# Optimization experiments

Hardware: AMD Instinct MI355X
Metric: run time of the kernel (lower is better)

Reference implementation:

```python
import jax, jax.numpy as jnp
import numpy as np

N_NODES = 40000
N_EDGES = 640000
D_IN = 128
D_OUT = 128


def setup_inputs() -> dict:
    key = jax.random.key(0)
    k_feat, k_src, k_dst, k_ws, k_wn = jax.random.split(key, 5)
    feat = jax.random.normal(k_feat, (N_NODES, D_IN), dtype=jnp.float32)
    src = jax.random.randint(k_src, (N_EDGES,), 0, N_NODES, dtype=jnp.int32)
    dst = jax.random.randint(k_dst, (N_EDGES,), 0, N_NODES, dtype=jnp.int32)
    # Glorot-ish init for the two dense layers
    scale = 1.0 / np.sqrt(D_IN)
    W_self = jax.random.normal(k_ws, (D_IN, D_OUT), dtype=jnp.float32) * scale
    W_neigh = jax.random.normal(k_wn, (D_IN, D_OUT), dtype=jnp.float32) * scale
    b_self = jnp.zeros((D_OUT,), dtype=jnp.float32)
    b_neigh = jnp.zeros((D_OUT,), dtype=jnp.float32)
    return {"feat": feat, "src": src, "dst": dst,
            "W_self": W_self, "b_self": b_self,
            "W_neigh": W_neigh, "b_neigh": b_neigh}


def reference(feat, src, dst, W_self, b_self, W_neigh, b_neigh):
    # --- mean aggregation: copy_src('h','m') + mean('m','neigh') ---
    # Gather source features along edges, segment-sum into dst, divide by in-degree.
    msgs = feat[src]  # [E, D_in]
    neigh_sum = jax.ops.segment_sum(msgs, dst, num_segments=N_NODES)  # [N, D_in]
    deg = jax.ops.segment_sum(jnp.ones((src.shape[0],), feat.dtype), dst,
                              num_segments=N_NODES)  # [N]
    # DGL mean reducer yields 0 for nodes with no incoming edges.
    h_neigh = neigh_sum / jnp.maximum(deg, 1.0)[:, None]
    # --- fc_self(h_self) + fc_neigh(h_neigh) ---
    rst = (feat @ W_self + b_self) + (h_neigh @ W_neigh + b_neigh)
    return rst
```

## Files before the change

### kernel.cpp

```cpp
#include <hip/hip_runtime.h>
#include <cstddef>

constexpr int NN  = 40000;
constexpr int NE  = 640000;
constexpr int DIM = 128;
constexpr int CAP = 48;
constexpr int PLANE = NN * 64;

typedef __attribute__((ext_vector_type(8))) short short8;
typedef __attribute__((ext_vector_type(4))) float floatx4;
typedef __attribute__((ext_vector_type(4))) unsigned int uint32x4;

__device__ __forceinline__ unsigned short f2bf(float x) {
    union { float f; unsigned int i; } v; v.f = x;
    unsigned int u = v.i;
    return (unsigned short)((u + 0x7fffu + ((u >> 16) & 1u)) >> 16);
}
__device__ __forceinline__ float bflo2f(unsigned int u) {
    union { unsigned int i; float f; } v; v.i = u << 16; return v.f;
}
__device__ __forceinline__ float bfhi2f(unsigned int u) {
    union { unsigned int i; float f; } v; v.i = u & 0xffff0000u; return v.f;
}

__global__ __launch_bounds__(256) void k_prep(
    const float* __restrict__ feat, const float* __restrict__ Wself,
    const float* __restrict__ Wneigh, unsigned short* __restrict__ featb,
    unsigned short* __restrict__ Wc, int* __restrict__ cnt)
{
    int b = blockIdx.x, t = threadIdx.x;
    if (b < 2500) {
        int idx8 = b * 256 + t;
        int n  = idx8 >> 4;
        int d0 = (idx8 & 15) << 3;
        const float4* fp =
            reinterpret_cast<const float4*>(feat + (size_t)n * DIM + d0);
        float4 v0 = fp[0], v1 = fp[1];
        unsigned int p0 = (unsigned int)f2bf(v0.x) | ((unsigned int)f2bf(v0.y) << 16);
        unsigned int p1 = (unsigned int)f2bf(v0.z) | ((unsigned int)f2bf(v0.w) << 16);
        unsigned int p2 = (unsigned int)f2bf(v1.x) | ((unsigned int)f2bf(v1.y) << 16);
        unsigned int p3 = (unsigned int)f2bf(v1.z) | ((unsigned int)f2bf(v1.w) << 16);
        int plane = d0 >> 6, off = d0 & 63;
        *reinterpret_cast<uint4*>(
            featb + (size_t)plane * PLANE + (size_t)n * 64 + off) =
            make_uint4(p0, p1, p2, p3);
    } else if (b < 2628) {
        int idx = (b - 2500) * 256 + t;
        int c = idx >> 13, n = (idx >> 6) & 127, kp = idx & 63;
        int k = c * 64 + kp;
        float w = (k < DIM) ? Wself[(size_t)k * DIM + n]
                            : Wneigh[(size_t)(k - DIM) * DIM + n];
        Wc[idx] = f2bf(w);
    } else {
        int i = (b - 2628) * 256 + t;
        if (i < NN) cnt[i] = 0;
    }
}

__global__ __launch_bounds__(256) void k_fill(
    const int* __restrict__ src, const int* __restrict__ dst,
    int* __restrict__ cnt, unsigned short* __restrict__ colf)
{
    int r  = blockIdx.x & 7;
    int bi = blockIdx.x >> 3;
    int lo = r * 5000, hi = lo + 5000;
    const uint32x4* d4 = reinterpret_cast<const uint32x4*>(dst) + (size_t)bi * 2000;
    const uint32x4* s4 = reinterpret_cast<const uint32x4*>(src) + (size_t)bi * 2000;
    for (int it = threadIdx.x; it < 2000; it += 256) {
        uint32x4 dv = __builtin_nontemporal_load(d4 + it);
        uint32x4 sv = __builtin_nontemporal_load(s4 + it);
        #pragma unroll
        for (int k = 0; k < 4; ++k) {
            int d = (int)dv[k];
            if (d >= lo && d < hi) {
                int pos = atomicAdd(&cnt[d], 1);
                if (pos < CAP) colf[d * CAP + pos] = (unsigned short)sv[k];
            }
        }
    }
}

__global__ __launch_bounds__(256) void k_gather(
    const unsigned int* __restrict__ fb32,
    const int* __restrict__ cnt,
    const unsigned short* __restrict__ colf,
    unsigned int* __restrict__ hnb32)
{
    int gtid = blockIdx.x * blockDim.x + threadIdx.x;
    int n = gtid >> 6;
    if (n >= NN) return;
    int lane = threadIdx.x & 63;

    int deg = cnt[n];
    int m = min(deg, CAP);
    int sv = (lane < m) ? (int)colf[n * CAP + lane] : 0;

    int vb = (lane >> 5) * (NN * 32) + (lane & 31);
    float ax0 = 0.f, ay0 = 0.f, ax1 = 0.f, ay1 = 0.f;
    int i = 0;
    for (; i + 7 < m; i += 8) {
        int s0 = __shfl(sv, i),     s1 = __shfl(sv, i + 1);
        int s2 = __shfl(sv, i + 2), s3 = __shfl(sv, i + 3);
        int s4 = __shfl(sv, i + 4), s5 = __shfl(sv, i + 5);
        int s6 = __shfl(sv, i + 6), s7 = __shfl(sv, i + 7);
        unsigned int u0 = fb32[vb + s0 * 32];
        unsigned int u1 = fb32[vb + s1 * 32];
        unsigned int u2 = fb32[vb + s2 * 32];
        unsigned int u3 = fb32[vb + s3 * 32];
        unsigned int u4 = fb32[vb + s4 * 32];
        unsigned int u5 = fb32[vb + s5 * 32];
        unsigned int u6 = fb32[vb + s6 * 32];
        unsigned int u7 = fb32[vb + s7 * 32];
        ax0 += bflo2f(u0); ay0 += bfhi2f(u0);
        ax1 += bflo2f(u1); ay1 += bfhi2f(u1);
        ax0 += bflo2f(u2); ay0 += bfhi2f(u2);
        ax1 += bflo2f(u3); ay1 += bfhi2f(u3);
        ax0 += bflo2f(u4); ay0 += bfhi2f(u4);
        ax1 += bflo2f(u5); ay1 += bfhi2f(u5);
        ax0 += bflo2f(u6); ay0 += bfhi2f(u6);
        ax1 += bflo2f(u7); ay1 += bfhi2f(u7);
    }
    for (; i + 3 < m; i += 4) {
        int s0 = __shfl(sv, i),     s1 = __shfl(sv, i + 1);
        int s2 = __shfl(sv, i + 2), s3 = __shfl(sv, i + 3);
        unsigned int u0 = fb32[vb + s0 * 32];
        unsigned int u1 = fb32[vb + s1 * 32];
        unsigned int u2 = fb32[vb + s2 * 32];
        unsigned int u3 = fb32[vb + s3 * 32];
        ax0 += bflo2f(u0); ay0 += bfhi2f(u0);
        ax1 += bflo2f(u1); ay1 += bfhi2f(u1);
        ax0 += bflo2f(u2); ay0 += bfhi2f(u2);
        ax1 += bflo2f(u3); ay1 += bfhi2f(u3);
    }
    for (; i < m; ++i) {
        int s0 = __shfl(sv, i);
        unsigned int u0 = fb32[vb + s0 * 32];
        ax0 += bflo2f(u0); ay0 += bfhi2f(u0);
    }
    float inv = 1.0f / fmaxf((float)deg, 1.0f);
    float ax = (ax0 + ax1) * inv, ay = (ay0 + ay1) * inv;
    hnb32[vb + n * 32] = (unsigned int)f2bf(ax) | ((unsigned int)f2bf(ay) << 16);
}

__global__ __launch_bounds__(320) void k_gemm(
    const unsigned short* __restrict__ featb,
    const unsigned short* __restrict__ hnb,
    const unsigned short* __restrict__ Wc,
    const float* __restrict__ bself, const float* __restrict__ bneigh,
    float* __restrict__ out)
{
    __shared__ unsigned short As[160 * 64];
    __shared__ unsigned short Bs[128 * 64];

    int t = threadIdx.x;
    int w = t >> 6;
    int lane = t & 63;
    int base_m = blockIdx.x * 160;

    floatx4 acc[2][8];
    #pragma unroll
    for (int a = 0; a < 2; ++a)
        #pragma unroll
        for (int b = 0; b < 8; ++b) acc[a][b] = (floatx4)0.f;

    for (int c = 0; c < 4; ++c) {
        const unsigned short* srcp =
            ((c < 2) ? featb + (size_t)c * PLANE
                     : hnb + (size_t)(c - 2) * PLANE) + (size_t)base_m * 64;
        #pragma unroll
        for (int it = 0; it < 4; ++it) {
            int s = t + it * 320;
            int m = s >> 3, g = s & 7;
            const unsigned short* sa = srcp + m * 64 + ((g ^ (m & 7)) << 3);
            __builtin_amdgcn_global_load_lds(
                (const __attribute__((address_space(1))) unsigned int*)sa,
                (__attribute__((address_space(3))) unsigned int*)(As + s * 8),
                16, 0, 0);
        }
        if (t < 256) {
            const unsigned short* bp = Wc + (size_t)c * 128 * 64;
            #pragma unroll
            for (int it = 0; it < 4; ++it) {
                int s = t + it * 256;
                int n = s >> 3, g = s & 7;
                const unsigned short* sb = bp + n * 64 + ((g ^ (n & 7)) << 3);
                __builtin_amdgcn_global_load_lds(
                    (const __attribute__((address_space(1))) unsigned int*)sb,
                    (__attribute__((address_space(3))) unsigned int*)(Bs + s * 8),
                    16, 0, 0);
            }
        }
        __syncthreads();

        #pragma unroll
        for (int sstep = 0; sstep < 2; ++sstep) {
            int gk = sstep * 4 + (lane >> 4);
            short8 af[2];
            #pragma unroll
            for (int mt = 0; mt < 2; ++mt) {
                int m = w * 32 + mt * 16 + (lane & 15);
                af[mt] = *reinterpret_cast<const short8*>(
                    As + m * 64 + ((gk ^ (m & 7)) << 3));
            }
            #pragma unroll
            for (int nt = 0; nt < 8; ++nt) {
                int n = nt * 16 + (lane & 15);
                short8 bf = *reinterpret_cast<const short8*>(
                    Bs + n * 64 + ((gk ^ (n & 7)) << 3));
                acc[0][nt] = __builtin_amdgcn_mfma_f32_16x16x32_bf16(
                    af[0], bf, acc[0][nt], 0, 0, 0);
                acc[1][nt] = __builtin_amdgcn_mfma_f32_16x16x32_bf16(
                    af[1], bf, acc[1][nt], 0, 0, 0);
            }
        }
        __syncthreads();
    }

    int colb = lane & 15;
    int quad = lane >> 4;
    #pragma unroll
    for (int nt = 0; nt < 8; ++nt) {
        int col = nt * 16 + colb;
        float bb = bself[col] + bneigh[col];
        #pragma unroll
        for (int mt = 0; mt < 2; ++mt) {
            #pragma unroll
            for (int r = 0; r < 4; ++r) {
                int row = base_m + w * 32 + mt * 16 + quad * 4 + r;
                out[(size_t)row * DIM + col] = acc[mt][nt][r] + bb;
            }
        }
    }
}

extern "C" void kernel_launch(void* const* d_in, const int* in_sizes, int n_in,
                              void* d_out, int out_size, void* d_ws, size_t ws_size,
                              hipStream_t stream)
{
    const float* feat   = (const float*)d_in[0];
    const int*   src    = (const int*)d_in[1];
    const int*   dst    = (const int*)d_in[2];
    const float* Wself  = (const float*)d_in[3];
    const float* bself  = (const float*)d_in[4];
    const float* Wneigh = (const float*)d_in[5];
    const float* bneigh = (const float*)d_in[6];
    float* out = (float*)d_out;

    char* ws = (char*)d_ws;
    unsigned short* featb = (unsigned short*)(ws);
    unsigned short* hnb   = (unsigned short*)(ws + 10240000);
    unsigned short* colf  = (unsigned short*)(ws + 20480000);
    unsigned short* Wc    = (unsigned short*)(ws + 24320000);
    int*            cnt   = (int*)(ws + 24385536);

    k_prep<<<2785, 256, 0, stream>>>(feat, Wself, Wneigh, featb, Wc, cnt);

    k_fill<<<640, 256, 0, stream>>>(src, dst, cnt, colf);

    k_gather<<<(NN * 64) / 256, 256, 0, stream>>>(
        (const unsigned int*)featb, cnt, colf, (unsigned int*)hnb);

    k_gemm<<<NN / 160, 320, 0, stream>>>(featb, hnb, Wc, bself, bneigh, out);
}
```

Before: 148.3 us.

## Replace global-atomic CSR fill with per-chunk LDS histogram, scan, and scatter

The single k_fill kernel, which used global atomics on the degree counters to place edges into fixed-capacity adjacency slots, becomes three kernels. k_hist builds per-chunk byte histograms of destinations in shared memory, k_scan does a column prefix sum across the 256 chunks to produce per-chunk base offsets and final degrees, and k_scat places edges using shared-memory atomics plus those bases. The aim is to remove contended global atomics. The cost is two extra launches, a 10MB histogram written and read back, and the assumption that a chunk's per-node count and its running offset fit in 8 bits.

```diff
diff --git a/kernel.cpp b/kernel.cpp
--- a/kernel.cpp
+++ b/kernel.cpp
@@ -6,10 +6,11 @@
 constexpr int DIM = 128;
 constexpr int CAP = 48;
 constexpr int PLANE = NN * 64;
+constexpr int NCH = 256;
+constexpr int ECH = NE / NCH;
 
 typedef __attribute__((ext_vector_type(8))) short short8;
 typedef __attribute__((ext_vector_type(4))) float floatx4;
-typedef __attribute__((ext_vector_type(4))) unsigned int uint32x4;
 
 __device__ __forceinline__ unsigned short f2bf(float x) {
     union { float f; unsigned int i; } v; v.f = x;
@@ -57,26 +58,92 @@
     }
 }
 
-__global__ __launch_bounds__(256) void k_fill(
+__global__ __launch_bounds__(256) void k_hist(
+    const int* __restrict__ dst, unsigned char* __restrict__ hist)
+{
+    __shared__ unsigned short d16[ECH];
+    __shared__ unsigned int   bins[10000];
+    int b = blockIdx.x, t = threadIdx.x;
+    const int* dp = dst + b * ECH;
+    for (int i = t; i < ECH; i += 256) d16[i] = (unsigned short)dp[i];
+    for (int q = 0; q < 4; ++q) {
+        int off = q * 10000;
+        for (int i = t; i < 10000; i += 256) bins[i] = 0;
+        __syncthreads();
+        for (int i = t; i < ECH; i += 256) {
+            int d = d16[i];
+            if (d >= off && d < off + 10000) atomicAdd(&bins[d - off], 1u);
+        }
+        __syncthreads();
+        for (int i = t; i < 2500; i += 256) {
+            unsigned int p = (bins[4*i] & 255u) | ((bins[4*i+1] & 255u) << 8)
+                           | ((bins[4*i+2] & 255u) << 16) | ((bins[4*i+3] & 255u) << 24);
+            *reinterpret_cast<unsigned int*>(
+                hist + (size_t)b * NN + off + 4 * i) = p;
+        }
+        __syncthreads();
+    }
+}
+
+__global__ __launch_bounds__(256) void k_scan(
+    unsigned char* __restrict__ hist, int* __restrict__ cnt)
+{
+    __shared__ unsigned char l[NCH * 200];
+    int n0 = blockIdx.x * 200, t = threadIdx.x;
+    unsigned int* lrow = reinterpret_cast<unsigned int*>(l + t * 200);
+    const unsigned int* rp =
+        reinterpret_cast<const unsigned int*>(hist + (size_t)t * NN + n0);
+    #pragma unroll
+    for (int i = 0; i < 50; ++i) lrow[i] = rp[i];
+    __syncthreads();
+    if (t < 200) {
+        int run = 0;
+        for (int b2 = 0; b2 < NCH; ++b2) {
+            int v = l[b2 * 200 + t];
+            l[b2 * 200 + t] = (unsigned char)run;
+            run += v;
+        }
+        cnt[n0 + t] = run;
+    }
+    __syncthreads();
+    unsigned int* wp = reinterpret_cast<unsigned int*>(hist + (size_t)t * NN + n0);
+    #pragma unroll
+    for (int i = 0; i < 50; ++i) wp[i] = lrow[i];
+}
+
+__global__ __launch_bounds__(256) void k_scat(
     const int* __restrict__ src, const int* __restrict__ dst,
-    int* __restrict__ cnt, unsigned short* __restrict__ colf)
-{
-    int r  = blockIdx.x & 7;
-    int bi = blockIdx.x >> 3;
-    int lo = r * 5000, hi = lo + 5000;
-    const uint32x4* d4 = reinterpret_cast<const uint32x4*>(dst) + (size_t)bi * 2000;
-    const uint32x4* s4 = reinterpret_cast<const uint32x4*>(src) + (size_t)bi * 2000;
-    for (int it = threadIdx.x; it < 2000; it += 256) {
-        uint32x4 dv = __builtin_nontemporal_load(d4 + it);
-        uint32x4 sv = __builtin_nontemporal_load(s4 + it);
-        #pragma unroll
-        for (int k = 0; k < 4; ++k) {
-            int d = (int)dv[k];
-            if (d >= lo && d < hi) {
-                int pos = atomicAdd(&cnt[d], 1);
-                if (pos < CAP) colf[d * CAP + pos] = (unsigned short)sv[k];
-            }
-        }
+    const unsigned char* __restrict__ base,
+    unsigned short* __restrict__ colf)
+{
+    __shared__ unsigned short d16[ECH];
+    __shared__ unsigned short s16[ECH];
+    __shared__ unsigned int   bins[10000];
+    __shared__ unsigned char  bq[10000];
+    int b = blockIdx.x, t = threadIdx.x;
+    const int* dp = dst + b * ECH;
+    const int* sp = src + b * ECH;
+    for (int i = t; i < ECH; i += 256) {
+        d16[i] = (unsigned short)dp[i];
+        s16[i] = (unsigned short)sp[i];
+    }
+    for (int q = 0; q < 4; ++q) {
+        int off = q * 10000;
+        for (int i = t; i < 10000; i += 256) bins[i] = 0;
+        const unsigned int* bp =
+            reinterpret_cast<const unsigned int*>(base + (size_t)b * NN + off);
+        unsigned int* bq32 = reinterpret_cast<unsigned int*>(bq);
+        for (int i = t; i < 2500; i += 256) bq32[i] = bp[i];
+        __syncthreads();
+        for (int i = t; i < ECH; i += 256) {
+            int d = d16[i];
+            if (d >= off && d < off + 10000) {
+                int lp  = (int)atomicAdd(&bins[d - off], 1u);
+                int pos = (int)bq[d - off] + lp;
+                if (pos < CAP) colf[d * CAP + pos] = s16[i];
+            }
+        }
+        __syncthreads();
     }
 }
 
@@ -252,10 +319,13 @@
     unsigned short* colf  = (unsigned short*)(ws + 20480000);
     unsigned short* Wc    = (unsigned short*)(ws + 24320000);
     int*            cnt   = (int*)(ws + 24385536);
+    unsigned char*  hist  = (unsigned char*)(ws + 24545536);
 
     k_prep<<<2785, 256, 0, stream>>>(feat, Wself, Wneigh, featb, Wc, cnt);
 
-    k_fill<<<640, 256, 0, stream>>>(src, dst, cnt, colf);
+    k_hist<<<NCH, 256, 0, stream>>>(dst, hist);
+    k_scan<<<NN / 200, 256, 0, stream>>>(hist, cnt);
+    k_scat<<<NCH, 256, 0, stream>>>(src, dst, hist, colf);
 
     k_gather<<<(NN * 64) / 256, 256, 0, stream>>>(
         (const unsigned int*)featb, cnt, colf, (unsigned int*)hnb);
```

New measurement: 171.3 us. 1.16x slower.
